# Kernel tuning notes

Hardware: AMD Instinct MI355X
Metric: run time of the kernel (lower is better)

Reference implementation:

```python
import jax, jax.numpy as jnp
import numpy as np

PATCH = 7      # level=2 -> patch_size = [None,5,7,9][2]
DIL = 2        # dilation_patch
PRED_K = 5     # level=2 -> pred_kernel_size = [None,3,5,5][2]


def conv2d(x, w, b=None, pad=0):
    y = jax.lax.conv_general_dilated(x, w, (1, 1), [(pad, pad), (pad, pad)],
                                     dimension_numbers=('NCHW', 'OIHW', 'NCHW'))
    if b is not None:
        y = y + b[None, :, None, None]
    return y


def deconv2d(x, w_t, stride=2, pad=1, groups=1):
    # torch ConvTranspose2d: weight layout [in, out/groups, kH, kW]
    # equivalent to lhs-dilated conv with spatially flipped, in/out-transposed kernel
    in_c, opg, kh, kw = w_t.shape
    w = w_t.reshape(groups, in_c // groups, opg, kh, kw)
    w = jnp.transpose(w, (0, 2, 1, 3, 4)).reshape(groups * opg, in_c // groups, kh, kw)
    w = w[:, :, ::-1, ::-1]
    p = kh - 1 - pad
    return jax.lax.conv_general_dilated(x, w, (1, 1), [(p, p), (p, p)],
                                        lhs_dilation=(stride, stride),
                                        dimension_numbers=('NCHW', 'OIHW', 'NCHW'),
                                        feature_group_count=groups)


def self_correlation(f):
    # SpatialCorrelationSampler(kernel_size=1, patch_size=PATCH, padding=0,
    #                           stride=1, dilation_patch=DIL), f correlated with itself.
    # Output flattened to [B, PATCH*PATCH, H, W], row-major over (di, dj).
    B, C, H, W = f.shape
    r = PATCH // 2
    pad = r * DIL
    fp = jnp.pad(f, ((0, 0), (0, 0), (pad, pad), (pad, pad)))
    outs = []
    for di in range(PATCH):
        for dj in range(PATCH):
            oy = (di - r) * DIL
            ox = (dj - r) * DIL
            sh = jax.lax.dynamic_slice(fp, (0, 0, pad + oy, pad + ox), (B, C, H, W))
            outs.append(jnp.sum(f * sh, axis=1))  # dot over channels
    return jnp.stack(outs, axis=1)


def warp(x, flow):
    # LiteFlowNet WarpingLayer with div_flow=1: bilinear grid_sample,
    # align_corners=True, zeros padding, then hard validity mask (>= 1.0).
    B, C, H, W = x.shape
    ys, xs = jnp.meshgrid(jnp.arange(H, dtype=x.dtype),
                          jnp.arange(W, dtype=x.dtype), indexing='ij')
    px = xs[None] + flow[:, 0]  # [B,H,W] pixel coords
    py = ys[None] + flow[:, 1]
    x0 = jnp.floor(px)
    y0 = jnp.floor(py)
    wx1 = px - x0
    wx0 = 1.0 - wx1
    wy1 = py - y0
    wy0 = 1.0 - wy1
    xf = x.reshape(B, C, H * W)

    def gather(xi, yi):
        valid = ((xi >= 0) & (xi <= W - 1) & (yi >= 0) & (yi <= H - 1)).astype(x.dtype)
        xc = jnp.clip(xi, 0, W - 1).astype(jnp.int32)
        yc = jnp.clip(yi, 0, H - 1).astype(jnp.int32)
        idx = (yc * W + xc).reshape(B, 1, H * W)
        v = jnp.take_along_axis(xf, idx, axis=2).reshape(B, C, H, W)
        return v * valid[:, None], valid

    v00, m00 = gather(x0, y0)
    v01, m01 = gather(x0 + 1.0, y0)
    v10, m10 = gather(x0, y0 + 1.0)
    v11, m11 = gather(x0 + 1.0, y0 + 1.0)
    out = (wy0[:, None] * (wx0[:, None] * v00 + wx1[:, None] * v01) +
           wy1[:, None] * (wx0[:, None] * v10 + wx1[:, None] * v11))
    msk = wy0 * (wx0 * m00 + wx1 * m01) + wy1 * (wx0 * m10 + wx1 * m11)
    mask = (msk >= 1.0).astype(x.dtype)[:, None]
    return out * mask


def setup_inputs() -> dict:
    key = jax.random.key(0)
    ks = jax.random.split(key, 12)
    B, C, H, W = 8, 128, 160, 160
    s = 0.05
    return {
        'feats': jax.random.normal(ks[0], (B, 2, C, H, W), jnp.float32),
        'flow': jax.random.normal(ks[1], (B, 2, H // 2, W // 2), jnp.float32) * 2.0,
        'conf': jax.random.uniform(ks[2], (B, 1, H // 2, W // 2), jnp.float32),
        'up_conf_w': jax.random.normal(ks[3], (1, 1, 4, 4), jnp.float32) * s,
        'up_flow_w': jax.random.normal(ks[4], (2, 1, 4, 4), jnp.float32) * s,
        'w1': jax.random.normal(ks[5], (128, PATCH * PATCH + 1, 3, 3), jnp.float32) * s,
        'b1': jnp.zeros((128,), jnp.float32),
        'w2': jax.random.normal(ks[6], (64, 128, 3, 3), jnp.float32) * s,
        'b2': jnp.zeros((64,), jnp.float32),
        'w3': jax.random.normal(ks[7], (32, 64, 3, 3), jnp.float32) * s,
        'b3': jnp.zeros((32,), jnp.float32),
        'disp_w': jax.random.normal(ks[8], (2, 32, PRED_K, PRED_K), jnp.float32) * s,
        'disp_b': jnp.zeros((2,), jnp.float32),
        'conf_w': jax.random.normal(ks[9], (1, 32, PRED_K, PRED_K), jnp.float32) * s,
        'conf_b': jnp.zeros((1,), jnp.float32),
    }


def reference(feats, flow, conf, up_conf_w, up_flow_w, w1, b1, w2, b2, w3, b3,
              disp_w, disp_b, conf_w, conf_b):
    lrelu = lambda v: jax.nn.leaky_relu(v, 0.1)
    conf = deconv2d(conf, up_conf_w, groups=1)          # [B,1,H,W]
    flow = deconv2d(flow, up_flow_w, groups=2)          # [B,2,H,W]
    corr = lrelu(self_correlation(feats[:, 0])) / feats.shape[2]
    x = jnp.concatenate([corr, conf], axis=1)           # [B,50,H,W]
    x = lrelu(conv2d(x, w1, b1, pad=1))
    x = lrelu(conv2d(x, w2, b2, pad=1))
    x = lrelu(conv2d(x, w3, b3, pad=1))
    disp = conv2d(x, disp_w, disp_b, pad=PRED_K // 2)   # [B,2,H,W]
    flow = warp(flow, disp)
    conf_out = jax.nn.sigmoid(conv2d(x, conf_w, conf_b, pad=PRED_K // 2))
    return flow, conf_out
```

## Files before the change

kernel.cpp:

```cpp
#include <hip/hip_runtime.h>
#include <math.h>

#define B 8
#define C 128
#define H 160
#define W 160
#define HW 25600
#define WP 162

typedef short bf16x8 __attribute__((ext_vector_type(8)));
typedef float f32x4  __attribute__((ext_vector_type(4)));

__device__ __forceinline__ unsigned short f2bf(float x) {
    union { float f; unsigned u; } v; v.f = x;
    unsigned r = v.u + 0x7fff + ((v.u >> 16) & 1);
    return (unsigned short)(r >> 16);
}
__device__ __forceinline__ float bf2f(unsigned short h) {
    union { unsigned u; float f; } v; v.u = ((unsigned)h) << 16;
    return v.f;
}

__device__ __forceinline__ void gload16(const unsigned short* g, unsigned short* l) {
    __builtin_amdgcn_global_load_lds(
        (const __attribute__((address_space(1))) void*)g,
        (__attribute__((address_space(3))) void*)l, 16, 0, 0);
}


__global__ void k_repack(const float* __restrict__ w1, const float* __restrict__ w2,
                         const float* __restrict__ w3, const float* __restrict__ dw,
                         const float* __restrict__ cw,
                         unsigned short* __restrict__ wpk1h, unsigned short* __restrict__ wpk1l,
                         unsigned short* __restrict__ wpk2h, unsigned short* __restrict__ wpk2l,
                         unsigned short* __restrict__ wpk3h, unsigned short* __restrict__ wpk3l,
                         float* __restrict__ wHT) {
    int idx = blockIdx.x * 256 + threadIdx.x;
    if (idx < 73728) {
        int t = idx / 8192; int r = idx % 8192; int co = r / 64; int ci = r % 64;
        float v = (ci < 50) ? w1[(co * 50 + ci) * 9 + t] : 0.f;
        unsigned short h = f2bf(v);
        wpk1h[idx] = h; wpk1l[idx] = f2bf(v - bf2f(h));
        return;
    }
    idx -= 73728;
    if (idx < 73728) {
        int t = idx / 8192; int r = idx % 8192; int co = r / 128; int ci = r % 128;
        float v = w2[(co * 128 + ci) * 9 + t];
        unsigned short h = f2bf(v);
        wpk2h[idx] = h; wpk2l[idx] = f2bf(v - bf2f(h));
        return;
    }
    idx -= 73728;
    if (idx < 18432) {
        int t = idx / 2048; int r = idx % 2048; int co = r / 64; int ci = r % 64;
        float v = w3[(co * 64 + ci) * 9 + t];
        unsigned short h = f2bf(v);
        wpk3h[idx] = h; wpk3l[idx] = f2bf(v - bf2f(h));
        return;
    }
    idx -= 18432;
    if (idx < 2400) {
        int ci = idx / 75; int rem = idx % 75; int k = rem / 3; int co = rem % 3;
        wHT[idx] = (co < 2) ? dw[(co * 32 + ci) * 25 + k] : cw[ci * 25 + k];
    }
}

__global__ void k_zeropad(unsigned short* __restrict__ xin, unsigned short* __restrict__ x1) {
    int idx = blockIdx.x * 256 + threadIdx.x;
    unsigned short* p; int C2;
    if (idx < 82432) { p = xin; C2 = 128; }
    else {
        idx -= 82432;
        if (idx >= 164864) return;
        p = x1; C2 = 256;
    }
    int chunks = C2 / 8;
    int percnt = 644 * chunks;
    int img = idx / percnt;
    int r = idx % percnt;
    int rp = r / chunks; int ch = r % chunks;
    int yy, xx;
    if (rp < 162)      { yy = 0;   xx = rp; }
    else if (rp < 324) { yy = 161; xx = rp - 162; }
    else { int s = rp - 324; yy = 1 + (s >> 1); xx = (s & 1) ? 161 : 0; }
    size_t off = ((size_t)(img * WP + yy) * WP + xx) * C2 + ch * 8;
    bf16x8 z = {0, 0, 0, 0, 0, 0, 0, 0};
    *(bf16x8*)&p[off] = z;
}

__global__ void k_upsample(const float* __restrict__ flow, const float* __restrict__ conf,
                           const float* __restrict__ up_flow_w, const float* __restrict__ up_conf_w,
                           float* __restrict__ flow_up, unsigned short* __restrict__ xin) {
    int idx = blockIdx.x * 256 + threadIdx.x;
    if (idx >= B * 3 * HW) return;
    int x = idx % W;
    int y = (idx / W) % H;
    int ch = (idx / HW) % 3;
    int b = idx / (3 * HW);
    const float* in;
    const float* w;
    if (ch < 2) { in = flow + (size_t)(b * 2 + ch) * 6400; w = up_flow_w + ch * 16; }
    else        { in = conf + (size_t)b * 6400;            w = up_conf_w; }
    float acc = 0.f;
#pragma unroll
    for (int dy = 0; dy < 4; ++dy) {
        int tny = y + 1 - dy;
        if (tny < 0 || (tny & 1)) continue;
        int iy = tny >> 1;
        if (iy >= 80) continue;
#pragma unroll
        for (int dx = 0; dx < 4; ++dx) {
            int tnx = x + 1 - dx;
            if (tnx < 0 || (tnx & 1)) continue;
            int ix = tnx >> 1;
            if (ix >= 80) continue;
            acc += in[iy * 80 + ix] * w[dy * 4 + dx];
        }
    }
    if (ch < 2) flow_up[(size_t)(b * 2 + ch) * HW + y * W + x] = acc;
    else {
        size_t off = ((size_t)(b * WP + y + 1) * WP + (x + 1)) * 128 + 64 + 17;
        unsigned short h = f2bf(acc);
        xin[off] = h;
        xin[off + 32] = f2bf(acc - bf2f(h));
    }
}

__global__ __launch_bounds__(256, 4) void k_corr(const float* __restrict__ feats,
                                                 unsigned short* __restrict__ xin) {
    const int bid = blockIdx.x;
    const int b = bid & 7;
    const int t = bid >> 3;
    const int x0 = (t % 5) * 32;
    const int y0 = (t / 5) * 8;
    const int tid = threadIdx.x;
    const int tx = tid & 31;
    const int ty = tid >> 5;
    __shared__ f32x4 sh[2][880];
    float acc[49];
#pragma unroll
    for (int i = 0; i < 49; ++i) acc[i] = 0.f;

    int soff[4]; bool sval[4];
#pragma unroll
    for (int s = 0; s < 4; ++s) {
        int i = tid + s * 256;
        int r = i / 44, cc = i % 44;
        int gy = y0 + r - 6, gx = x0 + cc - 6;
        sval[s] = (i < 880) && gy >= 0 && gy < H && gx >= 0 && gx < W;
        soff[s] = sval[s] ? (gy * W + gx) : 0;
    }
    const float* f = feats + (size_t)b * 2 * C * HW;
    f32x4 pre[4];
#pragma unroll
    for (int s = 0; s < 4; ++s)
#pragma unroll
        for (int c4 = 0; c4 < 4; ++c4)
            pre[s][c4] = sval[s] ? f[(size_t)c4 * HW + soff[s]] : 0.f;

    for (int cg = 0; cg < 32; ++cg) {
        f32x4* buf = sh[cg & 1];
#pragma unroll
        for (int s = 0; s < 4; ++s) {
            int i = tid + s * 256;
            if (i < 880) buf[i] = pre[s];
        }
        if (cg < 31) {
            const float* fn = f + (size_t)(cg + 1) * 4 * HW;
#pragma unroll
            for (int s = 0; s < 4; ++s)
#pragma unroll
                for (int c4 = 0; c4 < 4; ++c4)
                    pre[s][c4] = sval[s] ? fn[(size_t)c4 * HW + soff[s]] : 0.f;
        }
        __syncthreads();
        f32x4 ctr = buf[(ty + 6) * 44 + tx + 6];
#pragma unroll
        for (int dy = 0; dy < 7; ++dy) {
            const f32x4* row = &buf[(ty + 2 * dy) * 44 + tx];
#pragma unroll
            for (int dx = 0; dx < 7; ++dx) {
                f32x4 rv = row[2 * dx];
                float a = acc[dy * 7 + dx];
                a += ctr[0] * rv[0];
                a += ctr[1] * rv[1];
                a += ctr[2] * rv[2];
                a += ctr[3] * rv[3];
                acc[dy * 7 + dx] = a;
            }
        }
    }
    size_t pbase = ((size_t)(b * WP + y0 + ty + 1) * WP + (x0 + tx + 1)) * 128;
#pragma unroll
    for (int g = 0; g < 16; ++g) {
        bf16x8 pk;
#pragma unroll
        for (int e = 0; e < 8; ++e) {
            const int ch = ((g >> 3) * 32) + ((g & 3) * 8) + e;
            const int plane = (g >> 2) & 1;
            unsigned short os = 0;
            if (ch < 49) {
                float v = acc[ch];
                v = (v > 0.f) ? v : 0.1f * v;
                v *= 0.0078125f;
                unsigned short h = f2bf(v);
                os = plane ? f2bf(v - bf2f(h)) : h;
            }
            pk[e] = (short)os;
        }
        *(bf16x8*)&xin[pbase + g * 8] = pk;
    }
}

template<int CIN, int COUT, int COB, int NCO, int OUTF>
__global__ __launch_bounds__(256, 1) void k_convM(
    const unsigned short* __restrict__ in,
    const unsigned short* __restrict__ w_hi,  const unsigned short* __restrict__ w_lo,
    const float* __restrict__ bias,
    unsigned short* __restrict__ out_pk, float* __restrict__ out_f) {
    constexpr int NT = COB / 16;
    constexpr int NKC = CIN / 32;
    constexpr int CI2 = 2 * CIN;
    constexpr int WSZ = 9 * COB * 32;
    constexpr int GPP = 9 * COB * 4;
    constexpr int WCH = (2 * GPP) / 64;
    constexpr int ACH = (4 * 162 * 8) / 64;
    __shared__ __align__(128) unsigned short At[4 * 162 * 64];
    __shared__ __align__(128) unsigned short wl[2 * WSZ];

    const int bid = blockIdx.x;
    const int b = bid & 7;
    const int t = bid >> 3;
    const int co0 = (t % NCO) * COB;
    const int ybx = t / NCO;
    const int wave = threadIdx.x >> 6;
    const int lane = threadIdx.x & 63;
    const int rw = wave >> 1;
    const int x0w = (wave & 1) * 80;
    const int y = ybx * 2 + rw;
    const int m = lane & 15, q = lane >> 4;
    const int arow0 = b * WP + 2 * ybx;

    f32x4 acc[5][NT];
#pragma unroll
    for (int mt = 0; mt < 5; ++mt)
#pragma unroll
        for (int nt = 0; nt < NT; ++nt) acc[mt][nt] = (f32x4){0.f, 0.f, 0.f, 0.f};

    bf16x8 ah[2][5], al[2][5], bh[2][NT], bl[2][NT];

    for (int kc = 0; kc < NKC; ++kc) {
        __syncthreads();

#pragma unroll
        for (int k = 0; k < (ACH + 3) / 4; ++k) {
            int c = k * 4 + wave;
            if (c < ACH) {
                int ga = c * 64 + lane;
                int pl = ga >> 3;
                int r  = pl / 162;
                int px = pl - r * 162;
                int slot = (ga & 7) ^ (pl & 7);
                const unsigned short* src =
                    in + ((arow0 + r) * WP + px) * CI2 + kc * 64 + slot * 8;
                gload16(src, At + c * 512);
            }
        }
#pragma unroll
        for (int k = 0; k < WCH / 4; ++k) {
            int c = k * 4 + wave;
            int gw = c * 64 + lane;
            int p  = (c * 64) >= GPP;
            int idx = gw - p * GPP;
            int cc = idx >> 2, sl = idx & 3;
            int tap = cc / COB, co = cc % COB;
            int g = (sl - (co >> 1)) & 3;
            const unsigned short* wsrc =
                (p ? w_lo : w_hi) + (tap * COUT + co0 + co) * CIN + kc * 32 + g * 8;
            gload16(wsrc, wl + c * 512);
        }
        asm volatile("s_waitcnt vmcnt(0)" ::: "memory");
        __syncthreads();

#pragma unroll
        for (int mt = 0; mt < 5; ++mt) {
            int pl = rw * 162 + x0w + m + mt * 16;
            int g16 = (pl << 3) ^ (pl & 7) ^ q;
            ah[0][mt] = *(const bf16x8*)&At[g16 * 8];
            al[0][mt] = *(const bf16x8*)&At[(g16 ^ 4) * 8];
        }
#pragma unroll
        for (int nt = 0; nt < NT; ++nt) {
            const int co = nt * 16 + m;
            const int slot = (q + (co >> 1)) & 3;
            const int woff = co * 32 + slot * 8;
            bh[0][nt] = *(const bf16x8*)&wl[woff];
            bl[0][nt] = *(const bf16x8*)&wl[WSZ + woff];
        }

#pragma unroll
        for (int tap = 0; tap < 9; ++tap) {
            const int cur = tap & 1, nxt = cur ^ 1;
            if (tap < 8) {
                const int tap1 = tap + 1;
                const int dy = tap1 / 3, dx = tap1 % 3;
                const int plb = (rw + dy) * 162 + x0w + dx + m;
#pragma unroll
                for (int mt = 0; mt < 5; ++mt) {
                    int pl = plb + mt * 16;
                    int g16 = (pl << 3) ^ (pl & 7) ^ q;
                    ah[nxt][mt] = *(const bf16x8*)&At[g16 * 8];
                    al[nxt][mt] = *(const bf16x8*)&At[(g16 ^ 4) * 8];
                }
#pragma unroll
                for (int nt = 0; nt < NT; ++nt) {
                    const int co = nt * 16 + m;
                    const int slot = (q + (co >> 1)) & 3;
                    const int woff = (tap1 * COB + co) * 32 + slot * 8;
                    bh[nxt][nt] = *(const bf16x8*)&wl[woff];
                    bl[nxt][nt] = *(const bf16x8*)&wl[WSZ + woff];
                }
            }
#pragma unroll
            for (int nt = 0; nt < NT; ++nt) {
#pragma unroll
                for (int mt = 0; mt < 5; ++mt) {
                    acc[mt][nt] = __builtin_amdgcn_mfma_f32_16x16x32_bf16(ah[cur][mt], bh[cur][nt], acc[mt][nt], 0, 0, 0);
                    acc[mt][nt] = __builtin_amdgcn_mfma_f32_16x16x32_bf16(ah[cur][mt], bl[cur][nt], acc[mt][nt], 0, 0, 0);
                    acc[mt][nt] = __builtin_amdgcn_mfma_f32_16x16x32_bf16(al[cur][mt], bh[cur][nt], acc[mt][nt], 0, 0, 0);
                }
            }
        }
    }
#pragma unroll
    for (int nt = 0; nt < NT; ++nt) {
        const int co = co0 + nt * 16 + m;
        const float bv = bias[co];
#pragma unroll
        for (int mt = 0; mt < 5; ++mt) {
#pragma unroll
            for (int r = 0; r < 4; ++r) {
                float v = acc[mt][nt][r] + bv;
                v = (v > 0.f) ? v : 0.1f * v;
                const int x = x0w + mt * 16 + q * 4 + r;
                if (OUTF) {
                    out_f[((size_t)(b * COUT + co)) * HW + y * W + x] = v;
                } else {
                    const size_t off = ((size_t)(b * WP + y + 1) * WP + (x + 1)) * (2 * COUT)
                                     + ((co >> 5) * 64) + (co & 31);
                    unsigned short h = f2bf(v);
                    out_pk[off] = h;
                    out_pk[off + 32] = f2bf(v - bf2f(h));
                }
            }
        }
    }
}

__global__ __launch_bounds__(256) void k_head(const float* __restrict__ x3,
                                              const float* __restrict__ wHT,
                                              const float* __restrict__ disp_b,
                                              const float* __restrict__ conf_b,
                                              const float* __restrict__ flow_up,
                                              float* __restrict__ out) {
    const int bid = blockIdx.x;
    const int b = bid & 7;
    const int t = bid >> 3;
    const int x0 = (t % 10) * 16, y0 = (t / 10) * 16;
    const int tx = threadIdx.x & 15, ty = threadIdx.x >> 4;
    const int tid = threadIdx.x;
    __shared__ float sh[2 * 400];
    float a0 = 0.f, a1 = 0.f, a2 = 0.f;
    const float* xb = x3 + (size_t)(b * 32) * HW;
    for (int ci = 0; ci < 32; ci += 2) {
        __syncthreads();
        for (int i = tid; i < 800; i += 256) {
            int cc = i / 400;
            int rem = i - cc * 400;
            int r = rem / 20, c2 = rem % 20;
            int gy = y0 + r - 2, gx = x0 + c2 - 2;
            float v = 0.f;
            if (gy >= 0 && gy < H && gx >= 0 && gx < W)
                v = xb[(size_t)(ci + cc) * HW + gy * W + gx];
            sh[i] = v;
        }
        __syncthreads();
#pragma unroll
        for (int cc = 0; cc < 2; ++cc) {
            const float* t2 = sh + cc * 400;
            const float* wp = wHT + (size_t)(ci + cc) * 75;
#pragma unroll
            for (int k = 0; k < 25; ++k) {
                float v = t2[(ty + k / 5) * 20 + tx + (k % 5)];
                a0 += v * wp[k * 3 + 0];
                a1 += v * wp[k * 3 + 1];
                a2 += v * wp[k * 3 + 2];
            }
        }
    }
    const int gx = x0 + tx, gy = y0 + ty;
    float d0 = a0 + disp_b[0];
    float d1 = a1 + disp_b[1];
    float cf = a2 + conf_b[0];
    cf = 1.f / (1.f + expf(-cf));

    float px = (float)gx + d0, py = (float)gy + d1;
    float x0f = floorf(px), y0f = floorf(py);
    float wx1 = px - x0f, wx0 = 1.f - wx1;
    float wy1 = py - y0f, wy0 = 1.f - wy1;
    const float* f0 = flow_up + (size_t)(b * 2) * HW;
    const float* f1 = f0 + HW;

    float m00, m01, m10, m11;
    float a00, a01, a10, a11;
    float b00, b01, b10, b11;
    auto corner = [&](float xf, float yf, float& m, float& c0, float& c1) {
        bool valid = (xf >= 0.f) && (xf <= (float)(W - 1)) && (yf >= 0.f) && (yf <= (float)(H - 1));
        m = valid ? 1.f : 0.f;
        if (valid) {
            int xi = (int)xf, yi = (int)yf;
            int o = yi * W + xi;
            c0 = f0[o]; c1 = f1[o];
        } else { c0 = 0.f; c1 = 0.f; }
    };
    corner(x0f,       y0f,       m00, a00, b00);
    corner(x0f + 1.f, y0f,       m01, a01, b01);
    corner(x0f,       y0f + 1.f, m10, a10, b10);
    corner(x0f + 1.f, y0f + 1.f, m11, a11, b11);

    float o0 = wy0 * (wx0 * a00 + wx1 * a01) + wy1 * (wx0 * a10 + wx1 * a11);
    float o1 = wy0 * (wx0 * b00 + wx1 * b01) + wy1 * (wx0 * b10 + wx1 * b11);
    float msk = wy0 * (wx0 * m00 + wx1 * m01) + wy1 * (wx0 * m10 + wx1 * m11);
    float mask = (msk >= 1.f) ? 1.f : 0.f;

    int o = gy * W + gx;
    out[(size_t)(b * 2 + 0) * HW + o] = o0 * mask;
    out[(size_t)(b * 2 + 1) * HW + o] = o1 * mask;
    out[(size_t)B * 2 * HW + (size_t)b * HW + o] = cf;
}

extern "C" void kernel_launch(void* const* d_in, const int* in_sizes, int n_in,
                              void* d_out, int out_size, void* d_ws, size_t ws_size,
                              hipStream_t stream) {
    const float* feats     = (const float*)d_in[0];
    const float* flow      = (const float*)d_in[1];
    const float* conf      = (const float*)d_in[2];
    const float* up_conf_w = (const float*)d_in[3];
    const float* up_flow_w = (const float*)d_in[4];
    const float* w1        = (const float*)d_in[5];
    const float* b1        = (const float*)d_in[6];
    const float* w2        = (const float*)d_in[7];
    const float* b2        = (const float*)d_in[8];
    const float* w3        = (const float*)d_in[9];
    const float* b3        = (const float*)d_in[10];
    const float* disp_w    = (const float*)d_in[11];
    const float* disp_b    = (const float*)d_in[12];
    const float* conf_w    = (const float*)d_in[13];
    const float* conf_b    = (const float*)d_in[14];
    float* out = (float*)d_out;

    char* p = (char*)d_ws;
    const size_t SZ_XIN = (size_t)B * WP * WP * 128 * 2;
    const size_t SZ_X1  = (size_t)B * WP * WP * 256 * 2;
    unsigned short* xin = (unsigned short*)p;
    unsigned short* x1  = (unsigned short*)(p + SZ_XIN);
    char* p2 = p + SZ_XIN + SZ_X1;
    float* flow_up = (float*)p2;
    float* wHT     = (float*)(p2 + 1638400);
    unsigned short* wpk1h = (unsigned short*)(p2 + 1648000);
    unsigned short* wpk1l = wpk1h + 73728;
    unsigned short* wpk2h = wpk1l + 73728;
    unsigned short* wpk2l = wpk2h + 73728;
    unsigned short* wpk3h = wpk2l + 73728;
    unsigned short* wpk3l = wpk3h + 18432;
    unsigned short* x2 = xin;
    float* x3 = (float*)x1;

    k_repack<<<658, 256, 0, stream>>>(w1, w2, w3, disp_w, conf_w,
                                      wpk1h, wpk1l, wpk2h, wpk2l, wpk3h, wpk3l, wHT);
    k_zeropad<<<966, 256, 0, stream>>>(xin, x1);
    k_corr<<<800, 256, 0, stream>>>(feats, xin);
    k_upsample<<<(B * 3 * HW + 255) / 256, 256, 0, stream>>>(flow, conf, up_flow_w, up_conf_w,
                                                             flow_up, xin);
    k_convM<64, 128, 64, 2, 0><<<1280, 256, 0, stream>>>(xin, wpk1h, wpk1l, b1, x1, nullptr);
    k_convM<128, 64, 64, 1, 0><<<640, 256, 0, stream>>>(x1, wpk2h, wpk2l, b2, x2, nullptr);
    k_convM<64, 32, 32, 1, 1><<<640, 256, 0, stream>>>(x2, wpk3h, wpk3l, b3, nullptr, x3);
    k_head<<<800, 256, 0, stream>>>(x3, wHT, disp_b, conf_b, flow_up, out);
}
```

Before: 655.5 us.

## Load conv weights directly from global in MFMA fragment layout, shrink LDS tile

Weights are repacked into a fragment-ready layout so each lane reads its B operand straight from global memory (L2-cached), removing the weight LDS staging buffer. The activation tile drops its padding columns: horizontal halo loads are clamped and zeroed at the left and right edges, which shrinks LDS use. Launch bounds are raised to allow two blocks per CU. A missing __syncthreads is added in the correlation kernel loop. The cost is global-latency weight loads inside the tap loop and extra clamping logic.

```diff
diff --git a/kernel.cpp b/kernel.cpp
--- a/kernel.cpp
+++ b/kernel.cpp
@@ -40,7 +40,9 @@
         int t = idx / 8192; int r = idx % 8192; int co = r / 64; int ci = r % 64;
         float v = (ci < 50) ? w1[(co * 50 + ci) * 9 + t] : 0.f;
         unsigned short h = f2bf(v);
-        wpk1h[idx] = h; wpk1l[idx] = f2bf(v - bf2f(h));
+        int dst = ((t * 2 + (ci >> 5)) * 8 + (co >> 4)) * 512
+                + (((ci >> 3) & 3) * 16 + (co & 15)) * 8 + (ci & 7);
+        wpk1h[dst] = h; wpk1l[dst] = f2bf(v - bf2f(h));
         return;
     }
     idx -= 73728;
@@ -48,7 +50,9 @@
         int t = idx / 8192; int r = idx % 8192; int co = r / 128; int ci = r % 128;
         float v = w2[(co * 128 + ci) * 9 + t];
         unsigned short h = f2bf(v);
-        wpk2h[idx] = h; wpk2l[idx] = f2bf(v - bf2f(h));
+        int dst = ((t * 4 + (ci >> 5)) * 4 + (co >> 4)) * 512
+                + (((ci >> 3) & 3) * 16 + (co & 15)) * 8 + (ci & 7);
+        wpk2h[dst] = h; wpk2l[dst] = f2bf(v - bf2f(h));
         return;
     }
     idx -= 73728;
@@ -56,7 +60,9 @@
         int t = idx / 2048; int r = idx % 2048; int co = r / 64; int ci = r % 64;
         float v = w3[(co * 64 + ci) * 9 + t];
         unsigned short h = f2bf(v);
-        wpk3h[idx] = h; wpk3l[idx] = f2bf(v - bf2f(h));
+        int dst = ((t * 2 + (ci >> 5)) * 2 + (co >> 4)) * 512
+                + (((ci >> 3) & 3) * 16 + (co & 15)) * 8 + (ci & 7);
+        wpk3h[dst] = h; wpk3l[dst] = f2bf(v - bf2f(h));
         return;
     }
     idx -= 18432;
@@ -190,6 +196,7 @@
                 acc[dy * 7 + dx] = a;
             }
         }
+        __syncthreads();
     }
     size_t pbase = ((size_t)(b * WP + y0 + ty + 1) * WP + (x0 + tx + 1)) * 128;
 #pragma unroll
@@ -214,7 +221,7 @@
 }
 
 template<int CIN, int COUT, int COB, int NCO, int OUTF>
-__global__ __launch_bounds__(256, 1) void k_convM(
+__global__ __launch_bounds__(256, 2) void k_convM(
     const unsigned short* __restrict__ in,
     const unsigned short* __restrict__ w_hi,  const unsigned short* __restrict__ w_lo,
     const float* __restrict__ bias,
@@ -222,17 +229,14 @@
     constexpr int NT = COB / 16;
     constexpr int NKC = CIN / 32;
     constexpr int CI2 = 2 * CIN;
-    constexpr int WSZ = 9 * COB * 32;
-    constexpr int GPP = 9 * COB * 4;
-    constexpr int WCH = (2 * GPP) / 64;
-    constexpr int ACH = (4 * 162 * 8) / 64;
-    __shared__ __align__(128) unsigned short At[4 * 162 * 64];
-    __shared__ __align__(128) unsigned short wl[2 * WSZ];
+    constexpr int NCB = COUT / 16;
+    __shared__ __align__(128) unsigned short At[4 * 160 * 64];
 
     const int bid = blockIdx.x;
     const int b = bid & 7;
     const int t = bid >> 3;
     const int co0 = (t % NCO) * COB;
+    const int cb0 = co0 >> 4;
     const int ybx = t / NCO;
     const int wave = threadIdx.x >> 6;
     const int lane = threadIdx.x & 63;
@@ -241,6 +245,9 @@
     const int y = ybx * 2 + rw;
     const int m = lane & 15, q = lane >> 4;
     const int arow0 = b * WP + 2 * ybx;
+    const bool oobL = (x0w == 0) && (m == 0);
+    const bool oobR = (x0w == 80) && (m == 15);
+    const bf16x8 zf = {0, 0, 0, 0, 0, 0, 0, 0};
 
     f32x4 acc[5][NT];
 #pragma unroll
@@ -250,76 +257,58 @@
 
     bf16x8 ah[2][5], al[2][5], bh[2][NT], bl[2][NT];
 
+    auto lda = [&](int dy, int dx, bf16x8* dsth, bf16x8* dstl) {
+        const int tib = x0w + m + dx - 1;
+#pragma unroll
+        for (int mt = 0; mt < 5; ++mt) {
+            int ti = tib + mt * 16;
+            ti = ti < 0 ? 0 : (ti > 159 ? 159 : ti);
+            const int pl = (rw + dy) * 160 + ti;
+            const int g16 = (pl << 3) ^ (pl & 7) ^ q;
+            dsth[mt] = *(const bf16x8*)&At[g16 * 8];
+            dstl[mt] = *(const bf16x8*)&At[(g16 ^ 4) * 8];
+        }
+        if (dx == 0 && oobL) { dsth[0] = zf; dstl[0] = zf; }
+        if (dx == 2 && oobR) { dsth[4] = zf; dstl[4] = zf; }
+    };
+
     for (int kc = 0; kc < NKC; ++kc) {
         __syncthreads();
 
 #pragma unroll
-        for (int k = 0; k < (ACH + 3) / 4; ++k) {
+        for (int k = 0; k < 20; ++k) {
             int c = k * 4 + wave;
-            if (c < ACH) {
-                int ga = c * 64 + lane;
-                int pl = ga >> 3;
-                int r  = pl / 162;
-                int px = pl - r * 162;
-                int slot = (ga & 7) ^ (pl & 7);
-                const unsigned short* src =
-                    in + ((arow0 + r) * WP + px) * CI2 + kc * 64 + slot * 8;
-                gload16(src, At + c * 512);
-            }
-        }
-#pragma unroll
-        for (int k = 0; k < WCH / 4; ++k) {
-            int c = k * 4 + wave;
-            int gw = c * 64 + lane;
-            int p  = (c * 64) >= GPP;
-            int idx = gw - p * GPP;
-            int cc = idx >> 2, sl = idx & 3;
-            int tap = cc / COB, co = cc % COB;
-            int g = (sl - (co >> 1)) & 3;
-            const unsigned short* wsrc =
-                (p ? w_lo : w_hi) + (tap * COUT + co0 + co) * CIN + kc * 32 + g * 8;
-            gload16(wsrc, wl + c * 512);
+            int ga = c * 64 + lane;
+            int pl = ga >> 3;
+            int r  = pl / 160;
+            int px = pl - r * 160;
+            int slot = (ga & 7) ^ (pl & 7);
+            const unsigned short* src =
+                in + ((size_t)(arow0 + r) * WP + (px + 1)) * CI2 + kc * 64 + slot * 8;
+            gload16(src, At + c * 512);
+        }
+#pragma unroll
+        for (int nt = 0; nt < NT; ++nt) {
+            const int wb = ((0 * NKC + kc) * NCB + cb0 + nt) * 512 + lane * 8;
+            bh[0][nt] = *(const bf16x8*)&w_hi[wb];
+            bl[0][nt] = *(const bf16x8*)&w_lo[wb];
         }
         asm volatile("s_waitcnt vmcnt(0)" ::: "memory");
         __syncthreads();
 
-#pragma unroll
-        for (int mt = 0; mt < 5; ++mt) {
-            int pl = rw * 162 + x0w + m + mt * 16;
-            int g16 = (pl << 3) ^ (pl & 7) ^ q;
-            ah[0][mt] = *(const bf16x8*)&At[g16 * 8];
-            al[0][mt] = *(const bf16x8*)&At[(g16 ^ 4) * 8];
-        }
-#pragma unroll
-        for (int nt = 0; nt < NT; ++nt) {
-            const int co = nt * 16 + m;
-            const int slot = (q + (co >> 1)) & 3;
-            const int woff = co * 32 + slot * 8;
-            bh[0][nt] = *(const bf16x8*)&wl[woff];
-            bl[0][nt] = *(const bf16x8*)&wl[WSZ + woff];
-        }
+        lda(0, 0, ah[0], al[0]);
 
 #pragma unroll
         for (int tap = 0; tap < 9; ++tap) {
             const int cur = tap & 1, nxt = cur ^ 1;
             if (tap < 8) {
                 const int tap1 = tap + 1;
-                const int dy = tap1 / 3, dx = tap1 % 3;
-                const int plb = (rw + dy) * 162 + x0w + dx + m;
-#pragma unroll
-                for (int mt = 0; mt < 5; ++mt) {
-                    int pl = plb + mt * 16;
-                    int g16 = (pl << 3) ^ (pl & 7) ^ q;
-                    ah[nxt][mt] = *(const bf16x8*)&At[g16 * 8];
-                    al[nxt][mt] = *(const bf16x8*)&At[(g16 ^ 4) * 8];
-                }
+                lda(tap1 / 3, tap1 % 3, ah[nxt], al[nxt]);
 #pragma unroll
                 for (int nt = 0; nt < NT; ++nt) {
-                    const int co = nt * 16 + m;
-                    const int slot = (q + (co >> 1)) & 3;
-                    const int woff = (tap1 * COB + co) * 32 + slot * 8;
-                    bh[nxt][nt] = *(const bf16x8*)&wl[woff];
-                    bl[nxt][nt] = *(const bf16x8*)&wl[WSZ + woff];
+                    const int wb = ((tap1 * NKC + kc) * NCB + cb0 + nt) * 512 + lane * 8;
+                    bh[nxt][nt] = *(const bf16x8*)&w_hi[wb];
+                    bl[nxt][nt] = *(const bf16x8*)&w_lo[wb];
                 }
             }
 #pragma unroll
```

Measured after the change: 807.8 us. 1.23x slower.

## Shrink conv tiles to 32 channels and half-row width for two blocks per CU

Applied to the files above, without the earlier changes.

The MFMA conv kernel is retiled. Each block now covers 32 output channels and half the row width (80 px), and each wave owns one 16-channel slice with 5 M-tiles. This cuts LDS and register use so launch bounds allow two blocks per CU, and the grids grow 4x, 4x and 2x. In exchange the input halo and weights are loaded redundantly across more blocks. A missing __syncthreads is also added in the correlation loop, which closes an LDS reuse race.

```diff
diff --git a/kernel.cpp b/kernel.cpp
--- a/kernel.cpp
+++ b/kernel.cpp
@@ -190,6 +190,7 @@
                 acc[dy * 7 + dx] = a;
             }
         }
+        __syncthreads();
     }
     size_t pbase = ((size_t)(b * WP + y0 + ty + 1) * WP + (x0 + tx + 1)) * 128;
 #pragma unroll
@@ -213,62 +214,78 @@
     }
 }
 
-template<int CIN, int COUT, int COB, int NCO, int OUTF>
-__global__ __launch_bounds__(256, 1) void k_convM(
+template<int CIN, int COUT, int NCO, int OUTF>
+__global__ __launch_bounds__(256, 2) void k_convM(
     const unsigned short* __restrict__ in,
     const unsigned short* __restrict__ w_hi,  const unsigned short* __restrict__ w_lo,
     const float* __restrict__ bias,
     unsigned short* __restrict__ out_pk, float* __restrict__ out_f) {
-    constexpr int NT = COB / 16;
+    constexpr int COB = 32;
     constexpr int NKC = CIN / 32;
     constexpr int CI2 = 2 * CIN;
     constexpr int WSZ = 9 * COB * 32;
     constexpr int GPP = 9 * COB * 4;
-    constexpr int WCH = (2 * GPP) / 64;
-    constexpr int ACH = (4 * 162 * 8) / 64;
-    __shared__ __align__(128) unsigned short At[4 * 162 * 64];
+    __shared__ __align__(128) unsigned short At[4 * 82 * 64];
     __shared__ __align__(128) unsigned short wl[2 * WSZ];
 
     const int bid = blockIdx.x;
     const int b = bid & 7;
     const int t = bid >> 3;
     const int co0 = (t % NCO) * COB;
-    const int ybx = t / NCO;
+    const int xh  = (t / NCO) & 1;
+    const int ybx = t / (NCO * 2);
     const int wave = threadIdx.x >> 6;
     const int lane = threadIdx.x & 63;
-    const int rw = wave >> 1;
-    const int x0w = (wave & 1) * 80;
+    const int rw = wave & 1;
+    const int ch = wave >> 1;
     const int y = ybx * 2 + rw;
+    const int x0g = xh * 80;
     const int m = lane & 15, q = lane >> 4;
     const int arow0 = b * WP + 2 * ybx;
-
-    f32x4 acc[5][NT];
-#pragma unroll
-    for (int mt = 0; mt < 5; ++mt)
-#pragma unroll
-        for (int nt = 0; nt < NT; ++nt) acc[mt][nt] = (f32x4){0.f, 0.f, 0.f, 0.f};
-
-    bf16x8 ah[2][5], al[2][5], bh[2][NT], bl[2][NT];
+    const int coL = ch * 16 + m;
+
+    f32x4 acc[5];
+#pragma unroll
+    for (int mt = 0; mt < 5; ++mt) acc[mt] = (f32x4){0.f, 0.f, 0.f, 0.f};
+
+    bf16x8 ah[2][5], al[2][5], bh[2], bl[2];
+
+    auto lda = [&](int dy, int dx, bf16x8* dsth, bf16x8* dstl) {
+        const int cb = m + dx;
+#pragma unroll
+        for (int mt = 0; mt < 5; ++mt) {
+            const int pl = (rw + dy) * 82 + cb + mt * 16;
+            const int g16 = (pl << 3) ^ (pl & 7) ^ q;
+            dsth[mt] = *(const bf16x8*)&At[g16 * 8];
+            dstl[mt] = *(const bf16x8*)&At[(g16 ^ 4) * 8];
+        }
+    };
+    auto ldw = [&](int tap, bf16x8& h, bf16x8& l) {
+        const int slot = (q + (coL >> 1)) & 3;
+        const int woff = (tap * COB + coL) * 32 + slot * 8;
+        h = *(const bf16x8*)&wl[woff];
+        l = *(const bf16x8*)&wl[WSZ + woff];
+    };
 
     for (int kc = 0; kc < NKC; ++kc) {
         __syncthreads();
 
 #pragma unroll
-        for (int k = 0; k < (ACH + 3) / 4; ++k) {
+        for (int k = 0; k < 11; ++k) {
             int c = k * 4 + wave;
-            if (c < ACH) {
+            if (c < 41) {
                 int ga = c * 64 + lane;
                 int pl = ga >> 3;
-                int r  = pl / 162;
-                int px = pl - r * 162;
+                int r  = pl / 82;
+                int cx = pl - r * 82;
                 int slot = (ga & 7) ^ (pl & 7);
                 const unsigned short* src =
-                    in + ((arow0 + r) * WP + px) * CI2 + kc * 64 + slot * 8;
+                    in + ((size_t)(arow0 + r) * WP + x0g + cx) * CI2 + kc * 64 + slot * 8;
                 gload16(src, At + c * 512);
             }
         }
 #pragma unroll
-        for (int k = 0; k < WCH / 4; ++k) {
+        for (int k = 0; k < 9; ++k) {
             int c = k * 4 + wave;
             int gw = c * 64 + lane;
             int p  = (c * 64) >= GPP;
@@ -283,67 +300,35 @@
         asm volatile("s_waitcnt vmcnt(0)" ::: "memory");
         __syncthreads();
 
-#pragma unroll
-        for (int mt = 0; mt < 5; ++mt) {
-            int pl = rw * 162 + x0w + m + mt * 16;
-            int g16 = (pl << 3) ^ (pl & 7) ^ q;
-            ah[0][mt] = *(const bf16x8*)&At[g16 * 8];
-            al[0][mt] = *(const bf16x8*)&At[(g16 ^ 4) * 8];
-        }
-#pragma unroll
-        for (int nt = 0; nt < NT; ++nt) {
-            const int co = nt * 16 + m;
-            const int slot = (q + (co >> 1)) & 3;
-            const int woff = co * 32 + slot * 8;
-            bh[0][nt] = *(const bf16x8*)&wl[woff];
-            bl[0][nt] = *(const bf16x8*)&wl[WSZ + woff];
-        }
+        lda(0, 0, ah[0], al[0]);
+        ldw(0, bh[0], bl[0]);
 
 #pragma unroll
         for (int tap = 0; tap < 9; ++tap) {
             const int cur = tap & 1, nxt = cur ^ 1;
             if (tap < 8) {
                 const int tap1 = tap + 1;
-                const int dy = tap1 / 3, dx = tap1 % 3;
-                const int plb = (rw + dy) * 162 + x0w + dx + m;
-#pragma unroll
-                for (int mt = 0; mt < 5; ++mt) {
-                    int pl = plb + mt * 16;
-                    int g16 = (pl << 3) ^ (pl & 7) ^ q;
-                    ah[nxt][mt] = *(const bf16x8*)&At[g16 * 8];
-                    al[nxt][mt] = *(const bf16x8*)&At[(g16 ^ 4) * 8];
-                }
-#pragma unroll
-                for (int nt = 0; nt < NT; ++nt) {
-                    const int co = nt * 16 + m;
-                    const int slot = (q + (co >> 1)) & 3;
-                    const int woff = (tap1 * COB + co) * 32 + slot * 8;
-                    bh[nxt][nt] = *(const bf16x8*)&wl[woff];
-                    bl[nxt][nt] = *(const bf16x8*)&wl[WSZ + woff];
-                }
-            }
-#pragma unroll
-            for (int nt = 0; nt < NT; ++nt) {
-#pragma unroll
-                for (int mt = 0; mt < 5; ++mt) {
-                    acc[mt][nt] = __builtin_amdgcn_mfma_f32_16x16x32_bf16(ah[cur][mt], bh[cur][nt], acc[mt][nt], 0, 0, 0);
-                    acc[mt][nt] = __builtin_amdgcn_mfma_f32_16x16x32_bf16(ah[cur][mt], bl[cur][nt], acc[mt][nt], 0, 0, 0);
-                    acc[mt][nt] = __builtin_amdgcn_mfma_f32_16x16x32_bf16(al[cur][mt], bh[cur][nt], acc[mt][nt], 0, 0, 0);
-                }
-            }
-        }
-    }
-#pragma unroll
-    for (int nt = 0; nt < NT; ++nt) {
-        const int co = co0 + nt * 16 + m;
+                lda(tap1 / 3, tap1 % 3, ah[nxt], al[nxt]);
+                ldw(tap1, bh[nxt], bl[nxt]);
+            }
+#pragma unroll
+            for (int mt = 0; mt < 5; ++mt) {
+                acc[mt] = __builtin_amdgcn_mfma_f32_16x16x32_bf16(ah[cur][mt], bh[cur], acc[mt], 0, 0, 0);
+                acc[mt] = __builtin_amdgcn_mfma_f32_16x16x32_bf16(ah[cur][mt], bl[cur], acc[mt], 0, 0, 0);
+                acc[mt] = __builtin_amdgcn_mfma_f32_16x16x32_bf16(al[cur][mt], bh[cur], acc[mt], 0, 0, 0);
+            }
+        }
+    }
+    {
+        const int co = co0 + coL;
         const float bv = bias[co];
 #pragma unroll
         for (int mt = 0; mt < 5; ++mt) {
 #pragma unroll
             for (int r = 0; r < 4; ++r) {
-                float v = acc[mt][nt][r] + bv;
+                float v = acc[mt][r] + bv;
                 v = (v > 0.f) ? v : 0.1f * v;
-                const int x = x0w + mt * 16 + q * 4 + r;
+                const int x = x0g + mt * 16 + q * 4 + r;
                 if (OUTF) {
                     out_f[((size_t)(b * COUT + co)) * HW + y * W + x] = v;
                 } else {
@@ -483,8 +468,8 @@
     k_corr<<<800, 256, 0, stream>>>(feats, xin);
     k_upsample<<<(B * 3 * HW + 255) / 256, 256, 0, stream>>>(flow, conf, up_flow_w, up_conf_w,
                                                              flow_up, xin);
-    k_convM<64, 128, 64, 2, 0><<<1280, 256, 0, stream>>>(xin, wpk1h, wpk1l, b1, x1, nullptr);
-    k_convM<128, 64, 64, 1, 0><<<640, 256, 0, stream>>>(x1, wpk2h, wpk2l, b2, x2, nullptr);
-    k_convM<64, 32, 32, 1, 1><<<640, 256, 0, stream>>>(x2, wpk3h, wpk3l, b3, nullptr, x3);
+    k_convM<64, 128, 4, 0><<<5120, 256, 0, stream>>>(xin, wpk1h, wpk1l, b1, x1, nullptr);
+    k_convM<128, 64, 2, 0><<<2560, 256, 0, stream>>>(x1, wpk2h, wpk2l, b2, x2, nullptr);
+    k_convM<64, 32, 1, 1><<<1280, 256, 0, stream>>>(x2, wpk3h, wpk3l, b3, nullptr, x3);
     k_head<<<800, 256, 0, stream>>>(x3, wHT, disp_b, conf_b, flow_up, out);
 }
```

Result: slower. 678.8 us (+3.6%).
